# Performance work log

Measured on AMD Instinct MI355X. Metric: run time of the kernel, lower is better.

Reference implementation:

```python
import jax, jax.numpy as jnp
import numpy as np

B, N, K = 4096, 16384, 512

def setup_inputs() -> dict:
    key = jax.random.key(0)
    x = jax.random.normal(key, (B, N), dtype=jnp.float32)
    return {"x": x, "k": K}

def reference(x, k):
    # top-k of |x| along dim 1 (last dim for 2D x)
    _, top_idxs = jax.lax.top_k(jnp.abs(x), k)          # [B, k]
    rows = jnp.arange(x.shape[0])[:, None]               # [B, 1]
    mask = jnp.zeros(x.shape, dtype=bool).at[rows, top_idxs].set(True)
    return x * mask
```

## Files before the change

### kernel.cpp

```cpp
#include <hip/hip_runtime.h>

#define TPB 1024
#define NW (TPB / 64)
#define NCOLS 16384
#define F4PT (NCOLS / 4 / TPB)
#define NELEM (F4PT * 4)
#define BINS1 4096
#define TIE_CAP 2048

__device__ __forceinline__ unsigned keyOf(float f) {
    return __float_as_uint(f) & 0x7fffffffu;
}

template <int NBINS>
__device__ void suffix_select(const unsigned* hist, unsigned Krem,
                              unsigned* wsums, unsigned* bc) {
    const int t = threadIdx.x;
    const int lane = t & 63;
    const int wave = t >> 6;
    constexpr int CH = (NBINS + TPB - 1) / TPB;
    const int base = t * CH;
    unsigned hv[CH];
    unsigned c = 0;
#pragma unroll
    for (int i = 0; i < CH; ++i) {
        hv[i] = (base + i < NBINS) ? hist[base + i] : 0u;
        c += hv[i];
    }
    unsigned s = c;
#pragma unroll
    for (int off = 1; off < 64; off <<= 1) {
        unsigned o = __shfl_down(s, off);
        if (lane + off < 64) s += o;
    }
    if (lane == 0) wsums[wave] = s;
    __syncthreads();
    if (wave == 0) {
        unsigned ws = (lane < NW) ? wsums[lane] : 0u;
        unsigned ss = ws;
#pragma unroll
        for (int off = 1; off < 64; off <<= 1) {
            unsigned o = __shfl_down(ss, off);
            if (lane + off < 64) ss += o;
        }
        if (lane < NW) wsums[lane] = ss;
    }
    __syncthreads();
    unsigned gts = ((wave + 1 < NW) ? wsums[wave + 1] : 0u) + (s - c);
    if (gts < Krem && gts + c >= Krem) {
        unsigned cum = gts;
#pragma unroll
        for (int i = CH - 1; i >= 0; --i) {
            unsigned h = hv[i];
            cum += h;
            if (cum >= Krem) {
                bc[0] = (unsigned)(base + i);
                bc[1] = Krem - (cum - h);
                bc[2] = h;
                break;
            }
        }
    }
    __syncthreads();
}

__global__ __launch_bounds__(TPB) void topk_mask_kernel(
        const float* __restrict__ x, const int* __restrict__ kp,
        float* __restrict__ out) {
    __shared__ unsigned hist[BINS1];
    __shared__ unsigned wsums[NW];
    __shared__ unsigned bc[3];
    __shared__ unsigned tieIdx[TIE_CAP];
    __shared__ unsigned tieCnt;

    const int t = threadIdx.x;
    const unsigned K = (unsigned)(*kp);
    const size_t row = blockIdx.x;
    const float4* xr = reinterpret_cast<const float4*>(x) + row * (NCOLS / 4);
    float4* orow = reinterpret_cast<float4*>(out) + row * (NCOLS / 4);

    float vals[NELEM];
#pragma unroll
    for (int i = 0; i < F4PT; ++i) {
        float4 tmp = xr[t + i * TPB];
        vals[4 * i + 0] = tmp.x;
        vals[4 * i + 1] = tmp.y;
        vals[4 * i + 2] = tmp.z;
        vals[4 * i + 3] = tmp.w;
    }

    for (int i = t; i < BINS1; i += TPB) hist[i] = 0u;
    __syncthreads();
#pragma unroll
    for (int e = 0; e < NELEM; ++e) {
        unsigned key = keyOf(vals[e]);
        atomicAdd(&hist[key >> 19], 1u);
    }
    __syncthreads();
    suffix_select<BINS1>(hist, K, wsums, bc);
    const unsigned cut1 = bc[0];
    const unsigned r1 = bc[1];

    for (int i = t; i < BINS1; i += TPB) hist[i] = 0u;
    __syncthreads();
#pragma unroll
    for (int e = 0; e < NELEM; ++e) {
        unsigned key = keyOf(vals[e]);
        if ((key >> 19) == cut1) atomicAdd(&hist[(key >> 9) & 1023u], 1u);
    }
    __syncthreads();
    suffix_select<1024>(hist, r1, wsums, bc);
    const unsigned cut2 = bc[0];
    const unsigned r2 = bc[1];
    const unsigned pfx2 = (cut1 << 10) | cut2;

    for (int i = t; i < BINS1; i += TPB) hist[i] = 0u;
    __syncthreads();
#pragma unroll
    for (int e = 0; e < NELEM; ++e) {
        unsigned key = keyOf(vals[e]);
        if ((key >> 9) == pfx2) atomicAdd(&hist[key & 511u], 1u);
    }
    __syncthreads();
    suffix_select<512>(hist, r2, wsums, bc);
    const unsigned cut3 = bc[0];
    const unsigned r = bc[1];
    const unsigned E = bc[2];
    const unsigned T = (pfx2 << 9) | cut3;

    if (E > r) {
        if (t == 0) tieCnt = 0u;
        __syncthreads();
#pragma unroll
        for (int e = 0; e < NELEM; ++e) {
            if (keyOf(vals[e]) == T) {
                unsigned idx = (unsigned)((t + (e >> 2) * TPB) * 4 + (e & 3));
                unsigned p = atomicAdd(&tieCnt, 1u);
                if (p < TIE_CAP) tieIdx[p] = idx;
            }
        }
        __syncthreads();
        unsigned cnt = tieCnt < TIE_CAP ? tieCnt : TIE_CAP;
#pragma unroll
        for (int e = 0; e < NELEM; ++e) {
            if (keyOf(vals[e]) == T) {
                unsigned idx = (unsigned)((t + (e >> 2) * TPB) * 4 + (e & 3));
                unsigned rank = 0;
                for (unsigned p = 0; p < cnt; ++p) rank += (tieIdx[p] < idx) ? 1u : 0u;
                if (rank >= r) vals[e] = 0.0f;
            }
        }
        __syncthreads();
    }

#pragma unroll
    for (int i = 0; i < F4PT; ++i) {
        float4 o;
        o.x = (keyOf(vals[4 * i + 0]) >= T) ? vals[4 * i + 0] : 0.0f;
        o.y = (keyOf(vals[4 * i + 1]) >= T) ? vals[4 * i + 1] : 0.0f;
        o.z = (keyOf(vals[4 * i + 2]) >= T) ? vals[4 * i + 2] : 0.0f;
        o.w = (keyOf(vals[4 * i + 3]) >= T) ? vals[4 * i + 3] : 0.0f;
        orow[t + i * TPB] = o;
    }
}

extern "C" void kernel_launch(void* const* d_in, const int* in_sizes, int n_in,
                              void* d_out, int out_size, void* d_ws, size_t ws_size,
                              hipStream_t stream) {
    const float* x = (const float*)d_in[0];
    const int* kp = (const int*)d_in[1];
    float* out = (float*)d_out;
    const int rows = in_sizes[0] / NCOLS;
    topk_mask_kernel<<<rows, TPB, 0, stream>>>(x, kp, out);
}
```

Measured before the change: 130.6 us.

## Replace three-pass radix select with one histogram pass plus candidate rank sort

Widens the first histogram to 8192 bins, which spreads the boundary bucket thinner. When that bucket holds at most 1024 elements, the kernel gathers those candidates into shared memory and ranks them directly by all-pairs comparison, writing the kept positions to a bitmap. This replaces the second and third histogram passes and their barriers. A fallback keeps a two-level refinement with tie handling. The cost is an O(E^2) shared-memory rank loop, more shared memory per block, and a bitmap lookup in the output loop.

```diff
diff --git a/kernel.cpp b/kernel.cpp
--- a/kernel.cpp
+++ b/kernel.cpp
@@ -3,10 +3,11 @@
 #define TPB 1024
 #define NW (TPB / 64)
 #define NCOLS 16384
-#define F4PT (NCOLS / 4 / TPB)
-#define NELEM (F4PT * 4)
-#define BINS1 4096
-#define TIE_CAP 2048
+#define F4PT 4
+#define NELEM 16
+#define BINS1 8192
+#define SH1 18
+#define CAP 1024
 
 __device__ __forceinline__ unsigned keyOf(float f) {
     return __float_as_uint(f) & 0x7fffffffu;
@@ -20,13 +21,10 @@
     const int wave = t >> 6;
     constexpr int CH = (NBINS + TPB - 1) / TPB;
     const int base = t * CH;
-    unsigned hv[CH];
     unsigned c = 0;
 #pragma unroll
-    for (int i = 0; i < CH; ++i) {
-        hv[i] = (base + i < NBINS) ? hist[base + i] : 0u;
-        c += hv[i];
-    }
+    for (int i = 0; i < CH; ++i)
+        if (base + i < NBINS) c += hist[base + i];
     unsigned s = c;
 #pragma unroll
     for (int off = 1; off < 64; off <<= 1) {
@@ -49,9 +47,8 @@
     unsigned gts = ((wave + 1 < NW) ? wsums[wave + 1] : 0u) + (s - c);
     if (gts < Krem && gts + c >= Krem) {
         unsigned cum = gts;
-#pragma unroll
         for (int i = CH - 1; i >= 0; --i) {
-            unsigned h = hv[i];
+            unsigned h = hist[base + i];
             cum += h;
             if (cum >= Krem) {
                 bc[0] = (unsigned)(base + i);
@@ -64,14 +61,16 @@
     __syncthreads();
 }
 
-__global__ __launch_bounds__(TPB) void topk_mask_kernel(
+__global__ __launch_bounds__(TPB, 8) void topk_mask_kernel(
         const float* __restrict__ x, const int* __restrict__ kp,
         float* __restrict__ out) {
     __shared__ unsigned hist[BINS1];
+    __shared__ unsigned candKey[CAP];
+    __shared__ unsigned candIdx[CAP];
+    __shared__ unsigned bitmap[NCOLS / 32];
     __shared__ unsigned wsums[NW];
     __shared__ unsigned bc[3];
-    __shared__ unsigned tieIdx[TIE_CAP];
-    __shared__ unsigned tieCnt;
+    __shared__ unsigned cnt;
 
     const int t = threadIdx.x;
     const unsigned K = (unsigned)(*kp);
@@ -89,66 +88,84 @@
         vals[4 * i + 3] = tmp.w;
     }
 
-    for (int i = t; i < BINS1; i += TPB) hist[i] = 0u;
-    __syncthreads();
-#pragma unroll
-    for (int e = 0; e < NELEM; ++e) {
-        unsigned key = keyOf(vals[e]);
-        atomicAdd(&hist[key >> 19], 1u);
-    }
+#pragma unroll
+    for (int i = 0; i < BINS1 / TPB; ++i) hist[t + i * TPB] = 0u;
+    if (t < NCOLS / 32) bitmap[t] = 0u;
+    if (t == 0) cnt = 0u;
+    __syncthreads();
+
+#pragma unroll
+    for (int e = 0; e < NELEM; ++e)
+        atomicAdd(&hist[keyOf(vals[e]) >> SH1], 1u);
     __syncthreads();
     suffix_select<BINS1>(hist, K, wsums, bc);
     const unsigned cut1 = bc[0];
     const unsigned r1 = bc[1];
-
-    for (int i = t; i < BINS1; i += TPB) hist[i] = 0u;
-    __syncthreads();
-#pragma unroll
-    for (int e = 0; e < NELEM; ++e) {
-        unsigned key = keyOf(vals[e]);
-        if ((key >> 19) == cut1) atomicAdd(&hist[(key >> 9) & 1023u], 1u);
-    }
-    __syncthreads();
-    suffix_select<1024>(hist, r1, wsums, bc);
-    const unsigned cut2 = bc[0];
-    const unsigned r2 = bc[1];
-    const unsigned pfx2 = (cut1 << 10) | cut2;
-
-    for (int i = t; i < BINS1; i += TPB) hist[i] = 0u;
-    __syncthreads();
-#pragma unroll
-    for (int e = 0; e < NELEM; ++e) {
-        unsigned key = keyOf(vals[e]);
-        if ((key >> 9) == pfx2) atomicAdd(&hist[key & 511u], 1u);
-    }
-    __syncthreads();
-    suffix_select<512>(hist, r2, wsums, bc);
-    const unsigned cut3 = bc[0];
-    const unsigned r = bc[1];
     const unsigned E = bc[2];
-    const unsigned T = (pfx2 << 9) | cut3;
-
-    if (E > r) {
-        if (t == 0) tieCnt = 0u;
-        __syncthreads();
-#pragma unroll
-        for (int e = 0; e < NELEM; ++e) {
-            if (keyOf(vals[e]) == T) {
-                unsigned idx = (unsigned)((t + (e >> 2) * TPB) * 4 + (e & 3));
-                unsigned p = atomicAdd(&tieCnt, 1u);
-                if (p < TIE_CAP) tieIdx[p] = idx;
-            }
-        }
-        __syncthreads();
-        unsigned cnt = tieCnt < TIE_CAP ? tieCnt : TIE_CAP;
-#pragma unroll
-        for (int e = 0; e < NELEM; ++e) {
-            if (keyOf(vals[e]) == T) {
-                unsigned idx = (unsigned)((t + (e >> 2) * TPB) * 4 + (e & 3));
-                unsigned rank = 0;
-                for (unsigned p = 0; p < cnt; ++p) rank += (tieIdx[p] < idx) ? 1u : 0u;
-                if (rank >= r) vals[e] = 0.0f;
-            }
+
+    unsigned thrKey = 0;
+    const bool fastp = (E <= CAP);
+
+    if (fastp) {
+#pragma unroll
+        for (int e = 0; e < NELEM; ++e) {
+            unsigned key = keyOf(vals[e]);
+            if ((key >> SH1) == cut1) {
+                unsigned idx = 4u * (unsigned)(t + (e >> 2) * TPB) + (e & 3);
+                unsigned p = atomicAdd(&cnt, 1u);
+                candKey[p] = key;
+                candIdx[p] = idx;
+            }
+        }
+        __syncthreads();
+        for (unsigned p = t; p < E; p += TPB) {
+            unsigned key = candKey[p], idx = candIdx[p], rank = 0;
+            for (unsigned q = 0; q < E; ++q) {
+                unsigned ck = candKey[q];
+                rank += (ck > key) || (ck == key && candIdx[q] < idx);
+            }
+            if (rank < r1) atomicOr(&bitmap[idx >> 5], 1u << (idx & 31));
+        }
+        __syncthreads();
+    } else {
+        if (t < 1024) hist[t] = 0u;
+        __syncthreads();
+#pragma unroll
+        for (int e = 0; e < NELEM; ++e) {
+            unsigned key = keyOf(vals[e]);
+            if ((key >> SH1) == cut1) atomicAdd(&hist[(key >> 8) & 1023u], 1u);
+        }
+        __syncthreads();
+        suffix_select<1024>(hist, r1, wsums, bc);
+        const unsigned pfx = (cut1 << 10) | bc[0];
+        const unsigned r2 = bc[1];
+        if (t < 256) hist[t] = 0u;
+        __syncthreads();
+#pragma unroll
+        for (int e = 0; e < NELEM; ++e) {
+            unsigned key = keyOf(vals[e]);
+            if ((key >> 8) == pfx) atomicAdd(&hist[key & 255u], 1u);
+        }
+        __syncthreads();
+        suffix_select<256>(hist, r2, wsums, bc);
+        thrKey = (pfx << 8) | bc[0];
+        const unsigned rQ = bc[1];
+        if (t == 0) cnt = 0u;
+        __syncthreads();
+#pragma unroll
+        for (int e = 0; e < NELEM; ++e) {
+            if (keyOf(vals[e]) == thrKey) {
+                unsigned idx = 4u * (unsigned)(t + (e >> 2) * TPB) + (e & 3);
+                unsigned p = atomicAdd(&cnt, 1u);
+                if (p < CAP) candIdx[p] = idx;
+            }
+        }
+        __syncthreads();
+        unsigned m = cnt < CAP ? cnt : CAP;
+        for (unsigned p = t; p < m; p += TPB) {
+            unsigned idx = candIdx[p], rank = 0;
+            for (unsigned q = 0; q < m; ++q) rank += candIdx[q] < idx;
+            if (rank < rQ) atomicOr(&bitmap[idx >> 5], 1u << (idx & 31));
         }
         __syncthreads();
     }
@@ -156,10 +173,22 @@
 #pragma unroll
     for (int i = 0; i < F4PT; ++i) {
         float4 o;
-        o.x = (keyOf(vals[4 * i + 0]) >= T) ? vals[4 * i + 0] : 0.0f;
-        o.y = (keyOf(vals[4 * i + 1]) >= T) ? vals[4 * i + 1] : 0.0f;
-        o.z = (keyOf(vals[4 * i + 2]) >= T) ? vals[4 * i + 2] : 0.0f;
-        o.w = (keyOf(vals[4 * i + 3]) >= T) ? vals[4 * i + 3] : 0.0f;
+#pragma unroll
+        for (int j = 0; j < 4; ++j) {
+            float v = vals[4 * i + j];
+            unsigned key = keyOf(v);
+            unsigned idx = 4u * (unsigned)(t + i * TPB) + j;
+            bool keep;
+            if (fastp) {
+                unsigned b = key >> SH1;
+                keep = (b > cut1) ||
+                       (b == cut1 && ((bitmap[idx >> 5] >> (idx & 31)) & 1u));
+            } else {
+                keep = (key > thrKey) ||
+                       (key == thrKey && ((bitmap[idx >> 5] >> (idx & 31)) & 1u));
+            }
+            (&o.x)[j] = keep ? v : 0.0f;
+        }
         orow[t + i * TPB] = o;
     }
 }
```

Measured after the change: 153.8 us. +17.8%, slower.

## Stream row from memory per pass with small blocks and early-exit radix refinement

Applied to the files above, without the earlier changes.

The kernel no longer holds the whole row in registers. It drops to 256 threads per block with launch bounds targeting 8 blocks per SM, and re-reads the row from global memory (expected to hit in cache) on every pass. Radix refinement now stops once the boundary bucket holds at most 512 elements. Those candidates are ranked by key and index, the winners are marked in a shared bitmap, and the final writes use nontemporal stores. This trades register pressure and low occupancy for extra global reads of each row.

```diff
diff --git a/kernel.cpp b/kernel.cpp
--- a/kernel.cpp
+++ b/kernel.cpp
@@ -1,12 +1,14 @@
 #include <hip/hip_runtime.h>
 
-#define TPB 1024
+#define TPB 256
 #define NW (TPB / 64)
 #define NCOLS 16384
 #define F4PT (NCOLS / 4 / TPB)
-#define NELEM (F4PT * 4)
 #define BINS1 4096
-#define TIE_CAP 2048
+#define SH1 19
+#define CAP1 512
+
+typedef float f32x4 __attribute__((ext_vector_type(4)));
 
 __device__ __forceinline__ unsigned keyOf(float f) {
     return __float_as_uint(f) & 0x7fffffffu;
@@ -20,13 +22,10 @@
     const int wave = t >> 6;
     constexpr int CH = (NBINS + TPB - 1) / TPB;
     const int base = t * CH;
-    unsigned hv[CH];
     unsigned c = 0;
 #pragma unroll
-    for (int i = 0; i < CH; ++i) {
-        hv[i] = (base + i < NBINS) ? hist[base + i] : 0u;
-        c += hv[i];
-    }
+    for (int i = 0; i < CH; ++i)
+        if (base + i < NBINS) c += hist[base + i];
     unsigned s = c;
 #pragma unroll
     for (int off = 1; off < 64; off <<= 1) {
@@ -39,9 +38,9 @@
         unsigned ws = (lane < NW) ? wsums[lane] : 0u;
         unsigned ss = ws;
 #pragma unroll
-        for (int off = 1; off < 64; off <<= 1) {
+        for (int off = 1; off < NW; off <<= 1) {
             unsigned o = __shfl_down(ss, off);
-            if (lane + off < 64) ss += o;
+            if (lane + off < NW) ss += o;
         }
         if (lane < NW) wsums[lane] = ss;
     }
@@ -49,9 +48,9 @@
     unsigned gts = ((wave + 1 < NW) ? wsums[wave + 1] : 0u) + (s - c);
     if (gts < Krem && gts + c >= Krem) {
         unsigned cum = gts;
-#pragma unroll
         for (int i = CH - 1; i >= 0; --i) {
-            unsigned h = hv[i];
+            if (base + i >= NBINS) continue;
+            unsigned h = hist[base + i];
             cum += h;
             if (cum >= Krem) {
                 bc[0] = (unsigned)(base + i);
@@ -64,103 +63,124 @@
     __syncthreads();
 }
 
-__global__ __launch_bounds__(TPB) void topk_mask_kernel(
+__global__ __launch_bounds__(TPB, 8) void topk_mask_kernel(
         const float* __restrict__ x, const int* __restrict__ kp,
         float* __restrict__ out) {
     __shared__ unsigned hist[BINS1];
+    __shared__ unsigned bitmap[NCOLS / 32];
     __shared__ unsigned wsums[NW];
     __shared__ unsigned bc[3];
-    __shared__ unsigned tieIdx[TIE_CAP];
-    __shared__ unsigned tieCnt;
+    __shared__ unsigned cnt;
+
+    unsigned* candKey = hist;
+    unsigned* candIdx = hist + CAP1;
+    unsigned* hist2   = hist + 2 * CAP1;
 
     const int t = threadIdx.x;
     const unsigned K = (unsigned)(*kp);
-    const size_t row = blockIdx.x;
-    const float4* xr = reinterpret_cast<const float4*>(x) + row * (NCOLS / 4);
-    float4* orow = reinterpret_cast<float4*>(out) + row * (NCOLS / 4);
+    const float4* xr =
+        reinterpret_cast<const float4*>(x) + (size_t)blockIdx.x * (NCOLS / 4);
+    f32x4* orow =
+        reinterpret_cast<f32x4*>(out) + (size_t)blockIdx.x * (NCOLS / 4);
 
-    float vals[NELEM];
+    {
+        constexpr int ZH = BINS1 / TPB;
 #pragma unroll
+        for (int i = 0; i < ZH; ++i) hist[t * ZH + i] = 0u;
+        constexpr int ZB = (NCOLS / 32) / TPB;
+#pragma unroll
+        for (int i = 0; i < ZB; ++i) bitmap[t * ZB + i] = 0u;
+        if (t == 0) cnt = 0u;
+    }
+    __syncthreads();
+
+#pragma unroll 4
     for (int i = 0; i < F4PT; ++i) {
-        float4 tmp = xr[t + i * TPB];
-        vals[4 * i + 0] = tmp.x;
-        vals[4 * i + 1] = tmp.y;
-        vals[4 * i + 2] = tmp.z;
-        vals[4 * i + 3] = tmp.w;
-    }
-
-    for (int i = t; i < BINS1; i += TPB) hist[i] = 0u;
-    __syncthreads();
-#pragma unroll
-    for (int e = 0; e < NELEM; ++e) {
-        unsigned key = keyOf(vals[e]);
-        atomicAdd(&hist[key >> 19], 1u);
+        float4 v = xr[t + i * TPB];
+        atomicAdd(&hist[keyOf(v.x) >> SH1], 1u);
+        atomicAdd(&hist[keyOf(v.y) >> SH1], 1u);
+        atomicAdd(&hist[keyOf(v.z) >> SH1], 1u);
+        atomicAdd(&hist[keyOf(v.w) >> SH1], 1u);
     }
     __syncthreads();
     suffix_select<BINS1>(hist, K, wsums, bc);
-    const unsigned cut1 = bc[0];
-    const unsigned r1 = bc[1];
+    unsigned p = bc[0];
+    unsigned r = bc[1];
+    unsigned E = bc[2];
+    unsigned s = SH1;
 
-    for (int i = t; i < BINS1; i += TPB) hist[i] = 0u;
-    __syncthreads();
+    while (E > CAP1 && s > 0) {
+        unsigned sh2 = (s >= 8) ? (s - 8) : 0u;
+        unsigned width = s - sh2;
+        unsigned mask = (1u << width) - 1u;
+        if (t < 256) hist2[t] = 0u;
+        __syncthreads();
+#pragma unroll 2
+        for (int i = 0; i < F4PT; ++i) {
+            float4 v = xr[t + i * TPB];
 #pragma unroll
-    for (int e = 0; e < NELEM; ++e) {
-        unsigned key = keyOf(vals[e]);
-        if ((key >> 19) == cut1) atomicAdd(&hist[(key >> 9) & 1023u], 1u);
-    }
-    __syncthreads();
-    suffix_select<1024>(hist, r1, wsums, bc);
-    const unsigned cut2 = bc[0];
-    const unsigned r2 = bc[1];
-    const unsigned pfx2 = (cut1 << 10) | cut2;
-
-    for (int i = t; i < BINS1; i += TPB) hist[i] = 0u;
-    __syncthreads();
-#pragma unroll
-    for (int e = 0; e < NELEM; ++e) {
-        unsigned key = keyOf(vals[e]);
-        if ((key >> 9) == pfx2) atomicAdd(&hist[key & 511u], 1u);
-    }
-    __syncthreads();
-    suffix_select<512>(hist, r2, wsums, bc);
-    const unsigned cut3 = bc[0];
-    const unsigned r = bc[1];
-    const unsigned E = bc[2];
-    const unsigned T = (pfx2 << 9) | cut3;
-
-    if (E > r) {
-        if (t == 0) tieCnt = 0u;
-        __syncthreads();
-#pragma unroll
-        for (int e = 0; e < NELEM; ++e) {
-            if (keyOf(vals[e]) == T) {
-                unsigned idx = (unsigned)((t + (e >> 2) * TPB) * 4 + (e & 3));
-                unsigned p = atomicAdd(&tieCnt, 1u);
-                if (p < TIE_CAP) tieIdx[p] = idx;
+            for (int j = 0; j < 4; ++j) {
+                unsigned key = keyOf((&v.x)[j]);
+                if ((key >> s) == p) atomicAdd(&hist2[(key >> sh2) & mask], 1u);
             }
         }
         __syncthreads();
-        unsigned cnt = tieCnt < TIE_CAP ? tieCnt : TIE_CAP;
+        suffix_select<256>(hist2, r, wsums, bc);
+        p = (p << width) | bc[0];
+        r = bc[1];
+        E = bc[2];
+        s = sh2;
+    }
+
+    const bool keepAll = (r == E);
+    if (!keepAll) {
+#pragma unroll 2
+        for (int i = 0; i < F4PT; ++i) {
+            float4 v = xr[t + i * TPB];
 #pragma unroll
-        for (int e = 0; e < NELEM; ++e) {
-            if (keyOf(vals[e]) == T) {
-                unsigned idx = (unsigned)((t + (e >> 2) * TPB) * 4 + (e & 3));
-                unsigned rank = 0;
-                for (unsigned p = 0; p < cnt; ++p) rank += (tieIdx[p] < idx) ? 1u : 0u;
-                if (rank >= r) vals[e] = 0.0f;
+            for (int j = 0; j < 4; ++j) {
+                float f = (&v.x)[j];
+                unsigned key = keyOf(f);
+                if ((key >> s) == p) {
+                    unsigned idx = 4u * (unsigned)(t + i * TPB) + (unsigned)j;
+                    unsigned pos = atomicAdd(&cnt, 1u);
+                    if (pos < CAP1) { candKey[pos] = key; candIdx[pos] = idx; }
+                }
             }
+        }
+        __syncthreads();
+        unsigned m = (E < CAP1) ? E : CAP1;
+        for (unsigned q0 = t; q0 < m; q0 += TPB) {
+            unsigned k0 = candKey[q0], i0 = candIdx[q0], rank = 0;
+            for (unsigned q = 0; q < m; ++q) {
+                unsigned kq = candKey[q];
+                rank += (kq > k0) || (kq == k0 && candIdx[q] < i0);
+            }
+            if (rank < r) atomicOr(&bitmap[i0 >> 5], 1u << (i0 & 31));
         }
         __syncthreads();
     }
 
+#pragma unroll 2
+    for (int i = 0; i < F4PT; ++i) {
+        float4 v = xr[t + i * TPB];
+        f32x4 o;
 #pragma unroll
-    for (int i = 0; i < F4PT; ++i) {
-        float4 o;
-        o.x = (keyOf(vals[4 * i + 0]) >= T) ? vals[4 * i + 0] : 0.0f;
-        o.y = (keyOf(vals[4 * i + 1]) >= T) ? vals[4 * i + 1] : 0.0f;
-        o.z = (keyOf(vals[4 * i + 2]) >= T) ? vals[4 * i + 2] : 0.0f;
-        o.w = (keyOf(vals[4 * i + 3]) >= T) ? vals[4 * i + 3] : 0.0f;
-        orow[t + i * TPB] = o;
+        for (int j = 0; j < 4; ++j) {
+            float f = (&v.x)[j];
+            unsigned key = keyOf(f);
+            unsigned b = key >> s;
+            float of = 0.0f;
+            if (b > p) {
+                of = f;
+            } else if (b == p) {
+                unsigned idx = 4u * (unsigned)(t + i * TPB) + (unsigned)j;
+                if (keepAll || (((bitmap[idx >> 5] >> (idx & 31)) & 1u) != 0u))
+                    of = f;
+            }
+            o[j] = of;
+        }
+        __builtin_nontemporal_store(o, &orow[t + i * TPB]);
     }
 }
 
```

Measured after the change: 164.1 us. 1.26x slower.
